# Performance work log

Hardware: AMD Instinct MI355X
Metric: run time of the kernel (lower is better)

The kernel has to match this reference:

```python
import jax, jax.numpy as jnp
import numpy as np

B, T, A, P = 128, 128, 16, 4
D, H, Q, QI, V = 256, 512, 128, 512, 64
NUM_TRICKS = 13
SIGNAL_PHASE = 1
# static phase routing: contiguous blocks of T/P positions per phase (phase_mask buffer)
PHASE_ID = (np.arange(T) * P // T).astype(np.int32)
_DECAY = 0.6
_nt_left = NUM_TRICKS - np.arange(NUM_TRICKS, dtype=np.float32)
P_SIGNAL = ((1.0 - _DECAY) / (1.0 - _DECAY ** _nt_left)).astype(np.float32)


def setup_inputs() -> dict:
    key = jax.random.key(0)
    ks = jax.random.split(key, 12)
    a = jax.random.randint(ks[0], (B, T, A, 3), 0, V, dtype=jnp.int32)
    pad = (jax.random.uniform(ks[1], (B, T, A)) < 0.3) & (jnp.arange(A) >= 1)
    valid_actions = jnp.where(pad[..., None], -1, a)
    phase = jnp.broadcast_to(jnp.asarray(PHASE_ID), (B, T)).astype(jnp.int32)
    trick = jax.random.randint(ks[2], (B, T), 0, NUM_TRICKS, dtype=jnp.int32)
    backbone_embed = jax.random.normal(ks[3], (B, T, QI), jnp.float32)
    s = lambda k, shape, fan: jax.random.normal(k, shape, jnp.float32) / np.float32(np.sqrt(fan))
    return dict(
        backbone_embed=backbone_embed, valid_actions=valid_actions, phase=phase, trick=trick,
        emb0=s(ks[4], (V, D), D), emb1=s(ks[5], (V, D), D), emb2=s(ks[6], (V, D), D),
        ln_g=jnp.ones((D,), jnp.float32), ln_b=jnp.zeros((D,), jnp.float32),
        kW1=s(ks[7], (P, D, H), D), kb1=jnp.zeros((P, H), jnp.float32),
        kW2=s(ks[8], (P, H, H), H), kb2=jnp.zeros((P, H), jnp.float32),
        kW3=s(ks[9], (P, H, Q), H), kb3=jnp.zeros((P, Q), jnp.float32),
        qW=s(ks[10], (P, QI, Q), QI), qb=jnp.zeros((P, Q), jnp.float32),
    )


def _forward(backbone_embed, valid_actions, phase, trick,
             emb0, emb1, emb2, ln_g, ln_b,
             kW1, kb1, kW2, kb2, kW3, kb3, qW, qb):
    pid = PHASE_ID  # static (T,) routing -> gather per-position phase params (same math as mask gather/scatter)
    idx = jnp.clip(valid_actions, 0, V - 1)
    x = emb0[idx[..., 0]] + emb1[idx[..., 1]] + emb2[idx[..., 2]]  # (B,T,A,D) action embed
    mu = jnp.mean(x, -1, keepdims=True)
    var = jnp.var(x, -1, keepdims=True)
    x = (x - mu) * jax.lax.rsqrt(var + 1e-5) * ln_g + ln_b  # key LayerNorm
    # phase-branched key MLP (BranchedFF over MLP)
    h = jax.nn.relu(jnp.einsum('btad,tdh->btah', x, kW1[pid]) + kb1[pid][None, :, None, :])
    h = jax.nn.relu(jnp.einsum('btah,thg->btag', h, kW2[pid]) + kb2[pid][None, :, None, :])
    keyv = jnp.einsum('btah,thq->btaq', h, kW3[pid]) + kb3[pid][None, :, None, :]  # (B,T,A,Q)
    # phase-branched query Linear (BranchedFF over Linear)
    query = jnp.einsum('btd,tdq->btq', backbone_embed, qW[pid]) + qb[pid][None]  # (B,T,Q)
    attn = jnp.einsum('btq,btaq->bta', query, keyv) / np.float32(np.sqrt(Q))
    invalid = valid_actions[..., 0] == -1
    attn = jnp.where(invalid, -jnp.inf, attn)
    # no-signal log-weight
    n_valid = jnp.sum(~invalid, -1).astype(attn.dtype)  # (B,T)
    p_s = jnp.asarray(P_SIGNAL)[trick]
    wgt = jnp.log(jnp.maximum((1.0 - p_s) / p_s * (n_valid - 1.0), 1e-5))
    wgt = jnp.where(n_valid == 1.0, 0.0, wgt)
    attn = attn.at[..., 0].add(jnp.where(phase == SIGNAL_PHASE, wgt, 0.0))
    return jax.nn.log_softmax(attn, axis=-1)


def reference(backbone_embed, valid_actions, phase, trick,
              emb0, emb1, emb2, ln_g, ln_b,
              kW1, kb1, kW2, kb2, kW3, kb3, qW, qb):
    return _forward(backbone_embed, valid_actions, phase, trick,
                    emb0, emb1, emb2, ln_g, ln_b,
                    kW1, kb1, kW2, kb2, kW3, kb3, qW, qb)
```

## Files before the change

### kernel.cpp

```cpp
#include <hip/hip_runtime.h>
#include <hip/hip_bf16.h>
#include <cmath>

constexpr int Bc = 128, Tc = 128, Ac = 16;
constexpr int Dc = 256, Hc = 512, Qc = 128, QIc = 512, Vc = 64, NTk = 13;
constexpr float NEG_BIG = -1e30f;
constexpr float ACT_SCALE = 16.f;
constexpr float ACC_SCALE = 1.f / 256.f;
constexpr float ACC_TO_ACT = 1.f / 16.f;

typedef unsigned int uint;
typedef uint uint2v __attribute__((ext_vector_type(2)));
typedef int i32x8 __attribute__((ext_vector_type(8)));
typedef float f32x4 __attribute__((ext_vector_type(4)));

#define MFMA128(a, b, c) __builtin_amdgcn_mfma_scale_f32_16x16x128_f8f6f4( \
    (a), (b), (c), 0, 0, 0, 0x7F7F7F7F, 0, 0x7F7F7F7F)

__device__ __forceinline__ unsigned short f2bfu(float f) {
  __hip_bfloat16 h = __float2bfloat16(f);
  return *(unsigned short*)&h;
}
__device__ __forceinline__ float bf2f(short s) {
  return __uint_as_float(((unsigned)(unsigned short)s) << 16);
}
__device__ __forceinline__ uint pack4_fp8(float a, float b, float c, float d) {
  uint v = 0;
  v = __builtin_amdgcn_cvt_pk_fp8_f32(a, b, v, 0);
  v = __builtin_amdgcn_cvt_pk_fp8_f32(c, d, v, 1);
  return v;
}

__global__ void transform_all(const float* __restrict__ kW1, const float* __restrict__ kW2,
                              const float* __restrict__ kW3, const float* __restrict__ qW,
                              int* __restrict__ kW1f, int* __restrict__ kW2f,
                              int* __restrict__ kW3f, int* __restrict__ qWf) {
  int gid = blockIdx.x * 256 + threadIdx.x;
  const float* W;
  int* dst;
  int NT, KC, N, local;
  if (gid < 16384) {
    W = kW1; dst = kW1f; NT = 32; KC = 2; N = 512; local = gid;
  } else if (gid < 49152) {
    W = kW2; dst = kW2f; NT = 32; KC = 4; N = 512; local = gid - 16384;
  } else if (gid < 57344) {
    W = kW3; dst = kW3f; NT = 8; KC = 4; N = 128; local = gid - 49152;
  } else {
    W = qW; dst = qWf; NT = 8; KC = 4; N = 128; local = gid - 57344;
  }
  int lane = local & 63;
  int frag = local >> 6;
  int kc = frag % KC;
  int rest = frag / KC;
  int nt = rest % NT;
  int pp = rest / NT;
  int K = KC * 128;
  int n = nt * 16 + (lane & 15);
  int k0 = kc * 128 + (lane >> 4) * 32;
  const float* src = W + ((size_t)pp * K + k0) * N + n;
  i32x8 v;
#pragma unroll
  for (int jj = 0; jj < 8; ++jj) {
    float f0 = src[(size_t)(4 * jj + 0) * N] * ACT_SCALE;
    float f1 = src[(size_t)(4 * jj + 1) * N] * ACT_SCALE;
    float f2 = src[(size_t)(4 * jj + 2) * N] * ACT_SCALE;
    float f3 = src[(size_t)(4 * jj + 3) * N] * ACT_SCALE;
    v[jj] = (int)pack4_fp8(f0, f1, f2, f3);
  }
  *(i32x8*)(dst + (size_t)local * 8) = v;
}

template <int KC, int WT, int AT, bool RELU, int OUTMODE, int SIN, int SOUT, int CMASK>
__device__ __forceinline__ void layer128(
    const char* __restrict__ aB, void* __restrict__ o0,
    const int* __restrict__ Wfi, const float* __restrict__ bias,
    int wt0, int lane) {
  const int c = lane & 15, q = lane >> 4;
  const int sw = (c & 1) << 4;
  const char* ap = aB + (c & CMASK) * SIN + q * 32;

  f32x4 acc[WT][AT];
#pragma unroll
  for (int wt = 0; wt < WT; ++wt)
#pragma unroll
    for (int at = 0; at < AT; ++at)
#pragma unroll
      for (int r = 0; r < 4; ++r) acc[wt][at][r] = 0.f;

#pragma unroll 1
  for (int kc = 0; kc < KC; ++kc) {
    i32x8 bfr[AT];
#pragma unroll
    for (int at = 0; at < AT; ++at) {
      const char* pa = ap + at * 16 * SIN + kc * 128;
      uint4 u0 = *(const uint4*)(pa + sw);
      uint4 u1 = *(const uint4*)(pa + (16 ^ sw));
      i32x8 bv;
      bv[0] = (int)u0.x; bv[1] = (int)u0.y; bv[2] = (int)u0.z; bv[3] = (int)u0.w;
      bv[4] = (int)u1.x; bv[5] = (int)u1.y; bv[6] = (int)u1.z; bv[7] = (int)u1.w;
      bfr[at] = bv;
    }
#pragma unroll
    for (int wt = 0; wt < WT; ++wt) {
      const i32x8 wv = *(const i32x8*)(Wfi + ((size_t)((wt0 + wt) * KC + kc)) * 512 + lane * 8);
#pragma unroll
      for (int at = 0; at < AT; ++at)
        acc[wt][at] = MFMA128(wv, bfr[at], acc[wt][at]);
    }
  }

#pragma unroll
  for (int wt = 0; wt < WT; ++wt) {
    const int nb = (wt0 + wt) * 16 + 4 * q;
    float4 bv = *(const float4*)(bias + nb);
#pragma unroll
    for (int at = 0; at < AT; ++at) {
      const int row = at * 16 + c;
      if (OUTMODE == 0) {
        float s0 = fmaf(acc[wt][at][0], ACC_TO_ACT, bv.x * ACT_SCALE);
        float s1 = fmaf(acc[wt][at][1], ACC_TO_ACT, bv.y * ACT_SCALE);
        float s2 = fmaf(acc[wt][at][2], ACC_TO_ACT, bv.z * ACT_SCALE);
        float s3 = fmaf(acc[wt][at][3], ACC_TO_ACT, bv.w * ACT_SCALE);
        if (RELU) {
          s0 = fmaxf(s0, 0.f); s1 = fmaxf(s1, 0.f);
          s2 = fmaxf(s2, 0.f); s3 = fmaxf(s3, 0.f);
        }
        *(uint*)((char*)o0 + row * SOUT + (nb ^ sw)) = pack4_fp8(s0, s1, s2, s3);
      } else if (OUTMODE == 1) {
        float s0 = fmaf(acc[wt][at][0], ACC_SCALE, bv.x);
        float s1 = fmaf(acc[wt][at][1], ACC_SCALE, bv.y);
        float s2 = fmaf(acc[wt][at][2], ACC_SCALE, bv.z);
        float s3 = fmaf(acc[wt][at][3], ACC_SCALE, bv.w);
        uint2v u;
        u.x = ((uint)f2bfu(s1) << 16) | f2bfu(s0);
        u.y = ((uint)f2bfu(s3) << 16) | f2bfu(s2);
        *(uint2v*)((short*)o0 + row * SOUT + nb) = u;
      } else {
        if (c < 4) {
          float4 st;
          st.x = fmaf(acc[wt][at][0], ACC_SCALE, bv.x);
          st.y = fmaf(acc[wt][at][1], ACC_SCALE, bv.y);
          st.z = fmaf(acc[wt][at][2], ACC_SCALE, bv.z);
          st.w = fmaf(acc[wt][at][3], ACC_SCALE, bv.w);
          *(float4*)((float*)o0 + c * SOUT + nb) = st;
        }
      }
    }
  }
}

constexpr int SX = 288;
constexpr int SH = 544;
constexpr int SKV = 136;
constexpr int SQY = 132;

__global__ __launch_bounds__(512, 4) void policy_main(
    const float* __restrict__ be, const int* __restrict__ va,
    const int* __restrict__ phase, const int* __restrict__ trick,
    const float* __restrict__ emb0, const float* __restrict__ emb1,
    const float* __restrict__ emb2, const float* __restrict__ ln_g,
    const float* __restrict__ ln_b,
    const float* __restrict__ kb1, const float* __restrict__ kb2,
    const float* __restrict__ kb3, const float* __restrict__ qb,
    const int* __restrict__ kW1f, const int* __restrict__ kW2f,
    const int* __restrict__ kW3f, const int* __restrict__ qWf,
    float* __restrict__ out) {
  __shared__ __align__(16) char bufA[64 * SH];
  __shared__ __align__(16) char bufB[64 * SH];
  __shared__ __align__(16) char beAb[4 * SH];
  __shared__ __align__(16) float QYs[4 * SQY];
  __shared__ float attn_s[64];
  __shared__ int inval_s[64];
  __shared__ int ph_s[4], tr_s[4];

  char* Xs = bufA;
  char* H2 = bufA;
  char* H1 = bufB;
  short* KV = (short*)bufB;

  const int tid = threadIdx.x;
  const int lane = tid & 63;
  const int wu = __builtin_amdgcn_readfirstlane(tid >> 6);
  const int p = blockIdx.x & 3;
  const int g = blockIdx.x >> 2;
  const int b = g >> 3;
  const int t0 = p * 32 + (g & 7) * 4;
  const int bt0 = b * Tc + t0;

  if (tid < 64) {
    inval_s[tid] = (va[((size_t)bt0 * Ac + tid) * 3] == -1);
  } else if (tid < 68) {
    ph_s[tid - 64] = phase[bt0 + tid - 64];
  } else if (tid < 72) {
    tr_s[tid - 68] = trick[bt0 + tid - 68];
  }
  if (tid < 128) {
    const int tok = tid >> 5, li = tid & 31;
    const float4* bp4 = (const float4*)(be + ((size_t)(bt0 + tok)) * QIc + li * 16);
    float4 a0 = bp4[0], a1 = bp4[1], a2 = bp4[2], a3 = bp4[3];
    uint4 v;
    v.x = pack4_fp8(a0.x * ACT_SCALE, a0.y * ACT_SCALE, a0.z * ACT_SCALE, a0.w * ACT_SCALE);
    v.y = pack4_fp8(a1.x * ACT_SCALE, a1.y * ACT_SCALE, a1.z * ACT_SCALE, a1.w * ACT_SCALE);
    v.z = pack4_fp8(a2.x * ACT_SCALE, a2.y * ACT_SCALE, a2.z * ACT_SCALE, a2.w * ACT_SCALE);
    v.w = pack4_fp8(a3.x * ACT_SCALE, a3.y * ACT_SCALE, a3.z * ACT_SCALE, a3.w * ACT_SCALE);
    *(uint4*)(beAb + tok * SH + ((li * 16) ^ ((tok & 1) << 4))) = v;
  }
  {
    const int r = tid >> 3, part = tid & 7, d0 = part * 32;
    const int* vp = va + ((size_t)bt0 * Ac + r) * 3;
    int i0 = min(max(vp[0], 0), Vc - 1);
    int i1 = min(max(vp[1], 0), Vc - 1);
    int i2 = min(max(vp[2], 0), Vc - 1);
    const float4* e0 = (const float4*)(emb0 + i0 * Dc + d0);
    const float4* e1 = (const float4*)(emb1 + i1 * Dc + d0);
    const float4* e2 = (const float4*)(emb2 + i2 * Dc + d0);
    float xv[32];
    float sum = 0.f, ss = 0.f;
#pragma unroll
    for (int j = 0; j < 8; ++j) {
      float4 v0 = e0[j], v1 = e1[j], v2 = e2[j];
      float4 v;
      v.x = v0.x + v1.x + v2.x; v.y = v0.y + v1.y + v2.y;
      v.z = v0.z + v1.z + v2.z; v.w = v0.w + v1.w + v2.w;
      xv[j * 4 + 0] = v.x; xv[j * 4 + 1] = v.y; xv[j * 4 + 2] = v.z; xv[j * 4 + 3] = v.w;
      sum += v.x + v.y + v.z + v.w;
      ss += v.x * v.x + v.y * v.y + v.z * v.z + v.w * v.w;
    }
    sum += __shfl_xor(sum, 1); sum += __shfl_xor(sum, 2); sum += __shfl_xor(sum, 4);
    ss += __shfl_xor(ss, 1);   ss += __shfl_xor(ss, 2);   ss += __shfl_xor(ss, 4);
    const float mu = sum / (float)Dc;
    const float rstd = rsqrtf(ss / (float)Dc - mu * mu + 1e-5f);
    uint dw[8];
#pragma unroll
    for (int j = 0; j < 8; ++j) {
      float4 gg = *(const float4*)(ln_g + d0 + 4 * j);
      float4 bb = *(const float4*)(ln_b + d0 + 4 * j);
      float y0 = ((xv[4 * j + 0] - mu) * rstd * gg.x + bb.x) * ACT_SCALE;
      float y1 = ((xv[4 * j + 1] - mu) * rstd * gg.y + bb.y) * ACT_SCALE;
      float y2 = ((xv[4 * j + 2] - mu) * rstd * gg.z + bb.z) * ACT_SCALE;
      float y3 = ((xv[4 * j + 3] - mu) * rstd * gg.w + bb.w) * ACT_SCALE;
      dw[j] = pack4_fp8(y0, y1, y2, y3);
    }
    uint4 lo, hi;
    lo.x = dw[0]; lo.y = dw[1]; lo.z = dw[2]; lo.w = dw[3];
    hi.x = dw[4]; hi.y = dw[5]; hi.z = dw[6]; hi.w = dw[7];
    const int swr = (r & 1) << 4;
    *(uint4*)(Xs + r * SX + (d0 ^ swr)) = lo;
    *(uint4*)(Xs + r * SX + ((d0 + 16) ^ swr)) = hi;
  }
  __syncthreads();

  layer128<2, 2, 4, true, 0, SX, SH, 15>(Xs, H1, kW1f + (size_t)p * 32768,
                                         kb1 + p * Hc, wu * 2, lane);
  __builtin_amdgcn_sched_barrier(0);
  layer128<2, 2, 4, true, 0, SX, SH, 15>(Xs, H1, kW1f + (size_t)p * 32768,
                                         kb1 + p * Hc, 16 + wu * 2, lane);
  __syncthreads();

  layer128<4, 2, 4, true, 0, SH, SH, 15>(H1, H2, kW2f + (size_t)p * 65536,
                                         kb2 + p * Hc, wu * 2, lane);
  __builtin_amdgcn_sched_barrier(0);
  layer128<4, 2, 4, true, 0, SH, SH, 15>(H1, H2, kW2f + (size_t)p * 65536,
                                         kb2 + p * Hc, 16 + wu * 2, lane);
  __syncthreads();

  layer128<4, 1, 4, false, 1, SH, SKV, 15>(H2, (void*)KV, kW3f + (size_t)p * 16384,
                                           kb3 + p * Qc, wu, lane);
  __builtin_amdgcn_sched_barrier(0);
  layer128<4, 1, 1, false, 2, SH, SQY, 3>(beAb, (void*)QYs, qWf + (size_t)p * 16384,
                                          qb + p * Qc, wu, lane);
  __syncthreads();

  {
    const int r = tid >> 3, part = tid & 7, tok = r >> 4;
    const uint2v* kpu = (const uint2v*)(KV + r * SKV + part * 16);
    const float4* qp4 = (const float4*)(QYs + tok * SQY + part * 16);
    float s = 0.f;
#pragma unroll
    for (int j = 0; j < 4; ++j) {
      uint2v kk = kpu[j];
      float4 qq = qp4[j];
      s += bf2f((short)(kk.x & 0xffff)) * qq.x;
      s += bf2f((short)(kk.x >> 16)) * qq.y;
      s += bf2f((short)(kk.y & 0xffff)) * qq.z;
      s += bf2f((short)(kk.y >> 16)) * qq.w;
    }
    s += __shfl_xor(s, 1); s += __shfl_xor(s, 2); s += __shfl_xor(s, 4);
    if (part == 0) attn_s[r] = s * 0.08838834764831845f;
  }
  __syncthreads();

  if (tid < 4) {
    const int tok = tid;
    const int bt = bt0 + tok;
    float av[Ac];
    int nv = 0;
#pragma unroll
    for (int a = 0; a < Ac; ++a) {
      int iv = inval_s[tok * Ac + a];
      nv += iv ? 0 : 1;
      av[a] = iv ? NEG_BIG : attn_s[tok * Ac + a];
    }
    if (ph_s[tok] == 1) {
      const int nt = NTk - tr_s[tok];
      float dp = 1.f;
      for (int i = 0; i < nt; ++i) dp *= 0.6f;
      const float ps = 0.4f / (1.f - dp);
      float wgt = (nv == 1) ? 0.f : logf(fmaxf((1.f - ps) / ps * ((float)nv - 1.f), 1e-5f));
      av[0] += wgt;
    }
    float m = NEG_BIG;
#pragma unroll
    for (int a = 0; a < Ac; ++a) m = fmaxf(m, av[a]);
    float s = 0.f;
#pragma unroll
    for (int a = 0; a < Ac; ++a) s += expf(av[a] - m);
    const float lse = logf(s) + m;
#pragma unroll
    for (int a = 0; a < Ac; ++a)
      out[bt * Ac + a] = inval_s[tok * Ac + a] ? NEG_BIG : (av[a] - lse);
  }
}

extern "C" void kernel_launch(void* const* d_in, const int* in_sizes, int n_in,
                              void* d_out, int out_size, void* d_ws, size_t ws_size,
                              hipStream_t stream) {
  const float* be   = (const float*)d_in[0];
  const int*   va   = (const int*)d_in[1];
  const int*   ph   = (const int*)d_in[2];
  const int*   tr   = (const int*)d_in[3];
  const float* emb0 = (const float*)d_in[4];
  const float* emb1 = (const float*)d_in[5];
  const float* emb2 = (const float*)d_in[6];
  const float* lng  = (const float*)d_in[7];
  const float* lnb  = (const float*)d_in[8];
  const float* kW1  = (const float*)d_in[9];
  const float* kb1  = (const float*)d_in[10];
  const float* kW2  = (const float*)d_in[11];
  const float* kb2  = (const float*)d_in[12];
  const float* kW3  = (const float*)d_in[13];
  const float* kb3  = (const float*)d_in[14];
  const float* qW   = (const float*)d_in[15];
  const float* qb   = (const float*)d_in[16];
  float* out = (float*)d_out;

  int* kW1f = (int*)d_ws;
  int* kW2f = kW1f + 131072;
  int* kW3f = kW2f + 262144;
  int* qWf  = kW3f + 65536;

  transform_all<<<256, 256, 0, stream>>>(kW1, kW2, kW3, qW, kW1f, kW2f, kW3f, qWf);

  policy_main<<<4096, 512, 0, stream>>>(be, va, ph, tr, emb0, emb1, emb2, lng, lnb,
                                        kb1, kb2, kb3, qb, kW1f, kW2f, kW3f, qWf, out);
}
```

Before: 348.2 us.

## Software-pipeline MFMA operand loads and move query projection into first layer phase

Rewrites the inner GEMM loop of layer128 to double-buffer the LDS activation fragments and the global weight fragments, so the next operand load is issued before the current MFMAs. Small layers preload all weights up front. The query-projection layer is moved from the KV stage into the first-layer stage, and the sched_barriers between layer calls are dropped. Together these are meant to hide load latency and rebalance work across barrier phases, at the cost of more live registers and possible occupancy loss.

```diff
diff --git a/kernel.cpp b/kernel.cpp
--- a/kernel.cpp
+++ b/kernel.cpp
@@ -79,6 +79,18 @@
   const int sw = (c & 1) << 4;
   const char* ap = aB + (c & CMASK) * SIN + q * 32;
 
+#define LDB(kc_, at_) ({                                        \
+    const char* pa_ = ap + (at_) * 16 * SIN + (kc_) * 128;      \
+    uint4 u0_ = *(const uint4*)(pa_ + sw);                      \
+    uint4 u1_ = *(const uint4*)(pa_ + (16 ^ sw));               \
+    i32x8 bv_;                                                  \
+    bv_[0] = (int)u0_.x; bv_[1] = (int)u0_.y;                   \
+    bv_[2] = (int)u0_.z; bv_[3] = (int)u0_.w;                   \
+    bv_[4] = (int)u1_.x; bv_[5] = (int)u1_.y;                   \
+    bv_[6] = (int)u1_.z; bv_[7] = (int)u1_.w; bv_; })
+#define LDW(wt_, kc_) \
+    (*(const i32x8*)(Wfi + ((size_t)((wt0 + (wt_)) * KC + (kc_))) * 512 + lane * 8))
+
   f32x4 acc[WT][AT];
 #pragma unroll
   for (int wt = 0; wt < WT; ++wt)
@@ -87,27 +99,70 @@
 #pragma unroll
       for (int r = 0; r < 4; ++r) acc[wt][at][r] = 0.f;
 
-#pragma unroll 1
-  for (int kc = 0; kc < KC; ++kc) {
-    i32x8 bfr[AT];
-#pragma unroll
-    for (int at = 0; at < AT; ++at) {
-      const char* pa = ap + at * 16 * SIN + kc * 128;
-      uint4 u0 = *(const uint4*)(pa + sw);
-      uint4 u1 = *(const uint4*)(pa + (16 ^ sw));
-      i32x8 bv;
-      bv[0] = (int)u0.x; bv[1] = (int)u0.y; bv[2] = (int)u0.z; bv[3] = (int)u0.w;
-      bv[4] = (int)u1.x; bv[5] = (int)u1.y; bv[6] = (int)u1.z; bv[7] = (int)u1.w;
-      bfr[at] = bv;
-    }
-#pragma unroll
-    for (int wt = 0; wt < WT; ++wt) {
-      const i32x8 wv = *(const i32x8*)(Wfi + ((size_t)((wt0 + wt) * KC + kc)) * 512 + lane * 8);
-#pragma unroll
-      for (int at = 0; at < AT; ++at)
-        acc[wt][at] = MFMA128(wv, bfr[at], acc[wt][at]);
-    }
-  }
+  i32x8 bfA, bfB;
+  bfA = LDB(0, 0);
+
+  if constexpr (KC * WT <= 4) {
+    i32x8 wv[KC][WT];
+#pragma unroll
+    for (int kc = 0; kc < KC; ++kc)
+#pragma unroll
+      for (int wt = 0; wt < WT; ++wt) wv[kc][wt] = LDW(wt, kc);
+#pragma unroll
+    for (int kc = 0; kc < KC; ++kc) {
+#pragma unroll
+      for (int at = 0; at < AT; ++at) {
+        const int f = kc * AT + at;
+        const int nf = f + 1;
+        if ((f & 1) == 0) {
+          if (nf < KC * AT) bfB = LDB(nf / AT, nf % AT);
+#pragma unroll
+          for (int wt = 0; wt < WT; ++wt)
+            acc[wt][at] = MFMA128(wv[kc][wt], bfA, acc[wt][at]);
+        } else {
+          if (nf < KC * AT) bfA = LDB(nf / AT, nf % AT);
+#pragma unroll
+          for (int wt = 0; wt < WT; ++wt)
+            acc[wt][at] = MFMA128(wv[kc][wt], bfB, acc[wt][at]);
+        }
+      }
+      __builtin_amdgcn_sched_barrier(0);
+    }
+  } else {
+    i32x8 wvA[WT], wvB[WT];
+#pragma unroll
+    for (int wt = 0; wt < WT; ++wt) wvA[wt] = LDW(wt, 0);
+#pragma unroll
+    for (int kc = 0; kc < KC; ++kc) {
+      const bool ke = (kc & 1) == 0;
+      if (kc + 1 < KC) {
+#pragma unroll
+        for (int wt = 0; wt < WT; ++wt) {
+          if (ke) wvB[wt] = LDW(wt, kc + 1);
+          else    wvA[wt] = LDW(wt, kc + 1);
+        }
+      }
+#pragma unroll
+      for (int at = 0; at < AT; ++at) {
+        const int f = kc * AT + at;
+        const int nf = f + 1;
+        if ((f & 1) == 0) {
+          if (nf < KC * AT) bfB = LDB(nf / AT, nf % AT);
+#pragma unroll
+          for (int wt = 0; wt < WT; ++wt)
+            acc[wt][at] = MFMA128(ke ? wvA[wt] : wvB[wt], bfA, acc[wt][at]);
+        } else {
+          if (nf < KC * AT) bfA = LDB(nf / AT, nf % AT);
+#pragma unroll
+          for (int wt = 0; wt < WT; ++wt)
+            acc[wt][at] = MFMA128(ke ? wvA[wt] : wvB[wt], bfB, acc[wt][at]);
+        }
+      }
+      __builtin_amdgcn_sched_barrier(0);
+    }
+  }
+#undef LDB
+#undef LDW
 
 #pragma unroll
   for (int wt = 0; wt < WT; ++wt) {
@@ -252,23 +307,20 @@
 
   layer128<2, 2, 4, true, 0, SX, SH, 15>(Xs, H1, kW1f + (size_t)p * 32768,
                                          kb1 + p * Hc, wu * 2, lane);
-  __builtin_amdgcn_sched_barrier(0);
+  layer128<4, 1, 1, false, 2, SH, SQY, 3>(beAb, (void*)QYs, qWf + (size_t)p * 16384,
+                                          qb + p * Qc, wu, lane);
   layer128<2, 2, 4, true, 0, SX, SH, 15>(Xs, H1, kW1f + (size_t)p * 32768,
                                          kb1 + p * Hc, 16 + wu * 2, lane);
   __syncthreads();
 
   layer128<4, 2, 4, true, 0, SH, SH, 15>(H1, H2, kW2f + (size_t)p * 65536,
                                          kb2 + p * Hc, wu * 2, lane);
-  __builtin_amdgcn_sched_barrier(0);
   layer128<4, 2, 4, true, 0, SH, SH, 15>(H1, H2, kW2f + (size_t)p * 65536,
                                          kb2 + p * Hc, 16 + wu * 2, lane);
   __syncthreads();
 
   layer128<4, 1, 4, false, 1, SH, SKV, 15>(H2, (void*)KV, kW3f + (size_t)p * 16384,
                                            kb3 + p * Qc, wu, lane);
-  __builtin_amdgcn_sched_barrier(0);
-  layer128<4, 1, 1, false, 2, SH, SQY, 3>(beAb, (void*)QYs, qWf + (size_t)p * 16384,
-                                          qb + p * Qc, wu, lane);
   __syncthreads();
 
   {
```

Result: no change. 345.5 us (-0.8%).
